# Performance work log

Hardware: AMD Instinct MI355X
Metric: run time of the kernel (lower is better)

The kernel has to match this reference:

```python
import jax, jax.numpy as jnp
import numpy as np

EPS_NORM = 1e-10
EPS_EXP = 1e-6


def setup_inputs() -> dict:
    key = jax.random.key(0)
    k1, k2 = jax.random.split(key)
    B, F, H, W = 16, 2048, 8, 8
    X = jax.random.normal(k1, (B, F, H, W), dtype=jnp.float32)
    M = jax.random.normal(k2, (B, F, H, W), dtype=jnp.float32)
    return {"X": X, "M": M}


def reference(X, M):
    B, F, H, W = X.shape
    N = H * W
    X = X.reshape(B, F, N)
    M = M.reshape(B, F, N)

    # feature centering over dim=-2 (the feature axis of (B, F, N))
    X = X - X.mean(axis=1, keepdims=True)
    M = M - M.mean(axis=1, keepdims=True)

    # feature_normalize: L2 norm over dim 1, keepdim, + eps
    X = X / (jnp.linalg.norm(X, axis=1, keepdims=True) + EPS_NORM)
    M = M / (jnp.linalg.norm(M, axis=1, keepdims=True) + EPS_NORM)

    # MatmulTopkLoss: S = X @ M^T over spatial N -> (B, F, F)
    S = jnp.einsum('bfn,bgn->bfg', X, M)
    YX = S + jnp.transpose(S, (0, 2, 1))  # symmetrize
    P = jax.nn.softmax(YX, axis=-1)

    k = F // 2
    value, idx = jax.lax.top_k(P, k)  # (B, F, k) values desc, indices
    value_sum = value.sum(axis=-1, keepdims=True)
    row_pos = jnp.arange(F)[None, :, None]  # (1, F, 1)
    dist = jnp.abs(idx - row_pos).astype(value.dtype)
    C_xy = (value * dist / value_sum).mean(axis=-1)  # (B, F)

    xy = jnp.exp(-C_xy + C_xy.min() - EPS_EXP)
    return jnp.reshape(xy.mean(), (1,))
```

## Files before the change

### kernel.cpp

```cpp
#include <hip/hip_runtime.h>
#include <hip/hip_bf16.h>
#include <math.h>

#define B_   16
#define F_   2048
#define N_   64
#define K_   1024
#define YP   2056

typedef short bf16x8 __attribute__((ext_vector_type(8)));
typedef float v4f    __attribute__((ext_vector_type(4)));

__device__ __forceinline__ float wave_sum(float v) {
#pragma unroll
  for (int off = 32; off > 0; off >>= 1) v += __shfl_down(v, off, 64);
  return v;
}
__device__ __forceinline__ float wave_max(float v) {
#pragma unroll
  for (int off = 32; off > 0; off >>= 1) v = fmaxf(v, __shfl_down(v, off, 64));
  return v;
}

__device__ __forceinline__ unsigned f2bf(float x) {
  const unsigned u = __float_as_uint(x);
  return (u + 0x7FFFu + ((u >> 16) & 1u)) >> 16;
}
__device__ __forceinline__ float bf2f(unsigned us) {
  return __uint_as_float(us << 16);
}
__device__ __forceinline__ unsigned ord2u16(unsigned T) {
  return (T & 0x8000u) ? (T ^ 0x8000u) : (T ^ 0xFFFFu);
}
__device__ __forceinline__ unsigned ordpair(unsigned wd) {
  return wd ^ (0x80008000u | (((wd & 0x80008000u) >> 15) * 0x7FFFu));
}

__global__ __launch_bounds__(256) void stats_kernel(
    const float* __restrict__ X, const float* __restrict__ M,
    float* __restrict__ P) {
  __shared__ float red[4][N_][4];
  const int tid = threadIdx.x;
  const int b = blockIdx.x >> 4;
  const int fb = blockIdx.x & 15;
  const int f0 = fb * 128;
  const int fi = tid >> 6, n = tid & 63;
  float sx = 0.f, sxx = 0.f, sm = 0.f, smm = 0.f;
#pragma unroll 4
  for (int j = 0; j < 32; ++j) {
    const int f = f0 + fi + 4 * j;
    const size_t gi = ((size_t)b * F_ + f) * N_ + n;
    const float x = X[gi];
    const float m = M[gi];
    sx += x; sxx += x * x; sm += m; smm += m * m;
  }
  red[fi][n][0] = sx; red[fi][n][1] = sxx;
  red[fi][n][2] = sm; red[fi][n][3] = smm;
  __syncthreads();
  const int wn = tid & 63, word = tid >> 6;
  const float s = red[0][wn][word] + red[1][wn][word] +
                  red[2][wn][word] + red[3][wn][word];
  P[(((size_t)b * N_ + wn) * 4 + word) * 16 + fb] = s;
}

__global__ __launch_bounds__(256) void normbf_kernel(
    const float* __restrict__ X, const float* __restrict__ M,
    const float* __restrict__ P,
    short* __restrict__ Xb16, short* __restrict__ Mb16) {
  const int tid = threadIdx.x;
  const int b = blockIdx.x >> 4;
  const int f0 = (blockIdx.x & 15) * 128;
  const int n = tid & 63;
  const float* base = P + (((size_t)b * N_ + n) * 4) * 16;
  float acc4[4];
#pragma unroll
  for (int wj = 0; wj < 4; ++wj) {
    float s = 0.f;
#pragma unroll
    for (int i = 0; i < 16; ++i) s += base[16 * wj + i];
    acc4[wj] = s;
  }
  const float sx = acc4[0], sxx = acc4[1], sm = acc4[2], smm = acc4[3];
  const float mux = sx * (1.f / F_), mum = sm * (1.f / F_);
  const float rx = 1.f / (sqrtf(fmaxf(sxx - (float)F_ * mux * mux, 0.f)) + 1e-10f);
  const float rm = 1.f / (sqrtf(fmaxf(smm - (float)F_ * mum * mum, 0.f)) + 1e-10f);
#pragma unroll 4
  for (int jj = 0; jj < 32; ++jj) {
    const int f = f0 + (tid >> 6) + 4 * jj;
    const size_t gi = ((size_t)b * F_ + f) * N_ + n;
    Xb16[gi] = (short)f2bf((X[gi] - mux) * rx);
    Mb16[gi] = (short)f2bf((M[gi] - mum) * rm);
  }
}

__global__ __launch_bounds__(512)
__attribute__((amdgpu_waves_per_eu(4, 4)))
void rows_kernel(
    const short* __restrict__ Xb16, const short* __restrict__ Mb16,
    float* __restrict__ C) {
  __shared__ unsigned short yxu[16 * YP];
  __shared__ unsigned histS[8 * 256];

  const int tid = threadIdx.x;
  const int w = tid >> 6, lane = tid & 63;
  const int nl = lane & 15, q = lane >> 4;
  const int b = blockIdx.x >> 7;
  const int f0 = (blockIdx.x & 127) * 16;
  const int g0 = 256 * w;

  const short* __restrict__ Xb = Xb16 + (size_t)b * F_ * N_;
  const short* __restrict__ Mb = Mb16 + (size_t)b * F_ * N_;

  const short* Ax = Xb + (size_t)(f0 + nl) * N_ + 8 * q;
  const short* Am = Mb + (size_t)(f0 + nl) * N_ + 8 * q;
  const bf16x8 ax0 = *(const bf16x8*)(Ax);
  const bf16x8 ax1 = *(const bf16x8*)(Ax + 32);
  const bf16x8 am0 = *(const bf16x8*)(Am);
  const bf16x8 am1 = *(const bf16x8*)(Am + 32);

  v4f acc[16];
#pragma unroll
  for (int t = 0; t < 16; ++t) acc[t] = (v4f)(0.f);

#pragma unroll
  for (int t = 0; t < 16; ++t) {
    const short* Bm = Mb + (size_t)(g0 + 16 * t + nl) * N_ + 8 * q;
    const short* Bx = Xb + (size_t)(g0 + 16 * t + nl) * N_ + 8 * q;
    const bf16x8 bm0 = *(const bf16x8*)(Bm);
    const bf16x8 bm1 = *(const bf16x8*)(Bm + 32);
    const bf16x8 bx0 = *(const bf16x8*)(Bx);
    const bf16x8 bx1 = *(const bf16x8*)(Bx + 32);
    acc[t] = __builtin_amdgcn_mfma_f32_16x16x32_bf16(ax0, bm0, acc[t], 0, 0, 0);
    acc[t] = __builtin_amdgcn_mfma_f32_16x16x32_bf16(ax1, bm1, acc[t], 0, 0, 0);
    acc[t] = __builtin_amdgcn_mfma_f32_16x16x32_bf16(am0, bx0, acc[t], 0, 0, 0);
    acc[t] = __builtin_amdgcn_mfma_f32_16x16x32_bf16(am1, bx1, acc[t], 0, 0, 0);
  }

#pragma unroll
  for (int t = 0; t < 16; ++t) {
    const int col = g0 + 16 * t + nl;
#pragma unroll
    for (int r = 0; r < 4; ++r)
      yxu[(4 * q + r) * YP + col] = (unsigned short)f2bf(acc[t][r]);
  }
  __syncthreads();

  unsigned* wh = &histS[w << 8];
#pragma unroll 1
  for (int r4 = 0; r4 < 2; ++r4) {
    const int row = 2 * w + r4;
    const int frow = f0 + row;
    const uint4* rp = (const uint4*)(yxu + row * YP);

    unsigned pk[16];
    unsigned kmin = 0xFFFFFFFFu, kmax = 0u;
#pragma unroll
    for (int j = 0; j < 4; ++j) {
      const uint4 tt = rp[lane + 64 * j];
      const unsigned wds[4] = {tt.x, tt.y, tt.z, tt.w};
#pragma unroll
      for (int c = 0; c < 4; ++c) {
        const unsigned o = ordpair(wds[c]);
        pk[4 * j + c] = o;
        const unsigned o0 = o & 0xFFFFu, o1 = o >> 16;
        kmin = min(kmin, min(o0, o1));
        kmax = max(kmax, max(o0, o1));
      }
    }
#pragma unroll
    for (int off = 32; off > 0; off >>= 1) {
      kmin = min(kmin, (unsigned)__shfl_down((int)kmin, off, 64));
      kmax = max(kmax, (unsigned)__shfl_down((int)kmax, off, 64));
    }
    kmin = (unsigned)__shfl((int)kmin, 0, 64);
    kmax = (unsigned)__shfl((int)kmax, 0, 64);

    unsigned lo = kmin, R = kmax - kmin, krem = K_;
    unsigned T, tie_need;
    if (R == 0) {
      T = lo; tie_need = krem;
    } else {
      for (;;) {
        const int pos = 31 - __builtin_clz(R);
        const int sh = (pos > 7) ? (pos - 7) : 0;
#pragma unroll
        for (int i = 0; i < 4; ++i) wh[lane + 64 * i] = 0u;
        __builtin_amdgcn_wave_barrier();
#pragma unroll
        for (int c = 0; c < 16; ++c) {
          const unsigned o = pk[c];
          const unsigned d0 = (o & 0xFFFFu) - lo;
          const unsigned d1 = (o >> 16) - lo;
          if (d0 <= R) atomicAdd(&wh[d0 >> sh], 1u);
          if (d1 <= R) atomicAdd(&wh[d1 >> sh], 1u);
        }
        __builtin_amdgcn_wave_barrier();
        unsigned h[4];
#pragma unroll
        for (int i = 0; i < 4; ++i) h[i] = wh[4 * lane + i];
        unsigned s3 = h[3], s2 = h[2] + s3, s1 = h[1] + s2, s0 = h[0] + s1;
        unsigned tot = s0;
#pragma unroll
        for (int off = 1; off < 64; off <<= 1) {
          const unsigned v = __shfl_down(tot, off, 64);
          if (lane + off < 64) tot += v;
        }
        const unsigned above = tot - s0;
        const unsigned S[4] = {above + s0, above + s1, above + s2, above + s3};
        unsigned packed = 0;
        bool found = false;
#pragma unroll
        for (int i = 0; i < 4; ++i) {
          const unsigned Sip1 = S[i] - h[i];
          if (S[i] >= krem && Sip1 < krem) {
            packed = ((unsigned)(4 * lane + i) << 16) | Sip1;
            found = true;
          }
        }
        const unsigned long long bm = __ballot(found);
        const int winner = __ffsll(bm) - 1;
        packed = (unsigned)__shfl((int)packed, winner, 64);
        const unsigned D = packed >> 16;
        krem -= (packed & 0xFFFFu);
        if (sh == 0) { T = lo + D; tie_need = krem; break; }
        lo += (D << sh);
        R = (1u << sh) - 1u;
      }
    }

    float vs = 0.f, ws = 0.f;
    unsigned cnt[4];
#pragma unroll
    for (int j = 0; j < 4; ++j) {
      cnt[j] = 0;
#pragma unroll
      for (int c = 0; c < 4; ++c) {
        const unsigned o = pk[4 * j + c];
        const unsigned oo[2] = {o & 0xFFFFu, o >> 16};
#pragma unroll
        for (int i = 0; i < 2; ++i) {
          const int g = 512 * j + 8 * lane + 2 * c + i;
          if (oo[i] > T) {
            const float pv = __expf(bf2f(ord2u16(oo[i])));
            vs += pv; ws += pv * fabsf((float)(g - frow));
          } else if (oo[i] == T) cnt[j]++;
        }
      }
    }
    const float ptie = __expf(bf2f(ord2u16(T)));

    unsigned pA = cnt[0] | (cnt[1] << 16), pB = cnt[2] | (cnt[3] << 16);
    unsigned iA = pA, iB = pB;
#pragma unroll
    for (int off = 1; off < 64; off <<= 1) {
      const unsigned vA = __shfl_up(iA, off, 64);
      const unsigned vB = __shfl_up(iB, off, 64);
      if (lane >= off) { iA += vA; iB += vB; }
    }
    const unsigned eA = iA - pA, eB = iB - pB;
    const unsigned tA = (unsigned)__shfl((int)iA, 63, 64);
    const unsigned tB = (unsigned)__shfl((int)iB, 63, 64);
    unsigned G[4];
    G[0] = 0;
    G[1] = G[0] + (tA & 0xFFFFu);
    G[2] = G[1] + (tA >> 16);
    G[3] = G[2] + (tB & 0xFFFFu);
#pragma unroll
    for (int j = 0; j < 4; ++j) {
      if (cnt[j]) {
        const unsigned off = (j < 2) ? ((eA >> (16 * j)) & 0xFFFFu)
                                     : ((eB >> (16 * (j - 2))) & 0xFFFFu);
        unsigned cc = 0;
#pragma unroll
        for (int c = 0; c < 4; ++c) {
          const unsigned o = pk[4 * j + c];
          const unsigned oo[2] = {o & 0xFFFFu, o >> 16};
#pragma unroll
          for (int i = 0; i < 2; ++i) {
            if (oo[i] == T) {
              if (G[j] + off + cc < tie_need) {
                const int g = 512 * j + 8 * lane + 2 * c + i;
                vs += ptie; ws += ptie * fabsf((float)(g - frow));
              }
              cc++;
            }
          }
        }
      }
    }

    vs = wave_sum(vs); ws = wave_sum(ws);
    if (lane == 0)
      C[(size_t)b * F_ + frow] = (ws / vs) * (1.f / (float)K_);
  }
}

__global__ __launch_bounds__(1024) void final_kernel(
    const float* __restrict__ C, unsigned* __restrict__ out) {
  __shared__ float red[16];
  const int tid = threadIdx.x;
  const int wave = tid >> 6, lane = tid & 63;
  float v[32];
  float mn = 3.4e38f;
#pragma unroll
  for (int i = 0; i < 32; ++i) {
    v[i] = C[tid + 1024 * i];
    mn = fminf(mn, v[i]);
  }
  mn = -wave_max(-mn);
  if (lane == 0) red[wave] = mn;
  __syncthreads();
  float cmin = red[0];
  for (int w = 1; w < 16; ++w) cmin = fminf(cmin, red[w]);
  __syncthreads();
  float s = 0.f;
#pragma unroll
  for (int i = 0; i < 32; ++i) s += expf(cmin - v[i] - 1e-6f);
  s = wave_sum(s);
  if (lane == 0) red[wave] = s;
  __syncthreads();
  if (tid == 0) {
    float tot = 0.f;
    for (int w = 0; w < 16; ++w) tot += red[w];
    const float res = tot * (1.f / 32768.f);
    const __hip_bfloat16 hb = __float2bfloat16(res);
    const unsigned short u = *(const unsigned short*)&hb;
    out[0] = ((unsigned)u << 16) | (unsigned)u;
  }
}

extern "C" void kernel_launch(void* const* d_in, const int* in_sizes, int n_in,
                              void* d_out, int out_size, void* d_ws, size_t ws_size,
                              hipStream_t stream) {
  const float* X = (const float*)d_in[0];
  const float* M = (const float*)d_in[1];
  short* Xb16 = (short*)d_ws;
  short* Mb16 = Xb16 + (size_t)B_ * F_ * N_;
  float* C = (float*)(Mb16 + (size_t)B_ * F_ * N_);
  float* P = C + (size_t)B_ * F_;

  stats_kernel<<<dim3(B_ * 16), dim3(256), 0, stream>>>(X, M, P);
  normbf_kernel<<<dim3(B_ * 16), dim3(256), 0, stream>>>(X, M, P, Xb16, Mb16);
  rows_kernel<<<dim3(B_ * (F_ / 16)), dim3(512), 0, stream>>>(Xb16, Mb16, C);
  final_kernel<<<dim3(1), dim3(1024), 0, stream>>>(C, (unsigned*)d_out);
}
```

Before: 230.8 us.

## Interleave row pairs in LDS and vectorize stats/normalize with float4 loads

The rows kernel now packs two adjacent output rows into one 32-bit LDS word per column, so each wave reads its two rows with a single pass of uint4 loads. It computes min/max for both rows at once, then runs the radix select on the low or high half. The stats and normalize kernels switch to float4 loads and 4-wide bf16 stores, and normalize computes per-column mean and inverse norm once into shared memory. The aim is fewer LDS and global transactions, at the cost of 32 packed registers per lane in the rows kernel, which may raise register pressure.

New measurement: 239.7 us. 1.04x slower.

```diff
diff --git a/kernel.cpp b/kernel.cpp
--- a/kernel.cpp
+++ b/kernel.cpp
@@ -6,10 +6,11 @@
 #define F_   2048
 #define N_   64
 #define K_   1024
-#define YP   2056
+#define YPW  2052
 
 typedef short bf16x8 __attribute__((ext_vector_type(8)));
 typedef float v4f    __attribute__((ext_vector_type(4)));
+typedef unsigned short u16x4 __attribute__((ext_vector_type(4)));
 
 __device__ __forceinline__ float wave_sum(float v) {
 #pragma unroll
@@ -39,57 +40,98 @@
 __global__ __launch_bounds__(256) void stats_kernel(
     const float* __restrict__ X, const float* __restrict__ M,
     float* __restrict__ P) {
-  __shared__ float red[4][N_][4];
-  const int tid = threadIdx.x;
+  __shared__ float4 red[4][16][16];
+  const int t = threadIdx.x;
   const int b = blockIdx.x >> 4;
   const int fb = blockIdx.x & 15;
-  const int f0 = fb * 128;
-  const int fi = tid >> 6, n = tid & 63;
-  float sx = 0.f, sxx = 0.f, sm = 0.f, smm = 0.f;
-#pragma unroll 4
-  for (int j = 0; j < 32; ++j) {
-    const int f = f0 + fi + 4 * j;
-    const size_t gi = ((size_t)b * F_ + f) * N_ + n;
-    const float x = X[gi];
-    const float m = M[gi];
-    sx += x; sxx += x * x; sm += m; smm += m * m;
-  }
-  red[fi][n][0] = sx; red[fi][n][1] = sxx;
-  red[fi][n][2] = sm; red[fi][n][3] = smm;
-  __syncthreads();
-  const int wn = tid & 63, word = tid >> 6;
-  const float s = red[0][wn][word] + red[1][wn][word] +
-                  red[2][wn][word] + red[3][wn][word];
-  P[(((size_t)b * N_ + wn) * 4 + word) * 16 + fb] = s;
+  const int nq = t & 15, fr = t >> 4;
+  const float4* __restrict__ X4 = (const float4*)X;
+  const float4* __restrict__ M4 = (const float4*)M;
+  float4 sx = make_float4(0.f, 0.f, 0.f, 0.f), sxx = sx, sm = sx, smm = sx;
+#pragma unroll
+  for (int it = 0; it < 8; ++it) {
+    const int f = fb * 128 + fr + 16 * it;
+    const size_t idx = ((size_t)b * F_ + f) * 16 + nq;
+    const float4 x = X4[idx];
+    const float4 m = M4[idx];
+    sx.x += x.x; sx.y += x.y; sx.z += x.z; sx.w += x.w;
+    sxx.x += x.x * x.x; sxx.y += x.y * x.y;
+    sxx.z += x.z * x.z; sxx.w += x.w * x.w;
+    sm.x += m.x; sm.y += m.y; sm.z += m.z; sm.w += m.w;
+    smm.x += m.x * m.x; smm.y += m.y * m.y;
+    smm.z += m.z * m.z; smm.w += m.w * m.w;
+  }
+  red[0][fr][nq] = sx; red[1][fr][nq] = sxx;
+  red[2][fr][nq] = sm; red[3][fr][nq] = smm;
+  __syncthreads();
+  const int n = t & 63, word = t >> 6;
+  const int q2 = n >> 2, sub = n & 3;
+  float s = 0.f;
+#pragma unroll
+  for (int f2 = 0; f2 < 16; ++f2) {
+    const float4 v = red[word][f2][q2];
+    s += (sub == 0) ? v.x : (sub == 1) ? v.y : (sub == 2) ? v.z : v.w;
+  }
+  P[(((size_t)b * N_ + n) * 4 + word) * 16 + fb] = s;
 }
 
 __global__ __launch_bounds__(256) void normbf_kernel(
     const float* __restrict__ X, const float* __restrict__ M,
     const float* __restrict__ P,
     short* __restrict__ Xb16, short* __restrict__ Mb16) {
-  const int tid = threadIdx.x;
+  __shared__ float der[N_][4];
+  __shared__ float sums[N_][4];
+  const int t = threadIdx.x;
   const int b = blockIdx.x >> 4;
   const int f0 = (blockIdx.x & 15) * 128;
-  const int n = tid & 63;
-  const float* base = P + (((size_t)b * N_ + n) * 4) * 16;
-  float acc4[4];
-#pragma unroll
-  for (int wj = 0; wj < 4; ++wj) {
+  {
+    const int n = t & 63, word = t >> 6;
+    const float* base = P + (((size_t)b * N_ + n) * 4 + word) * 16;
     float s = 0.f;
 #pragma unroll
-    for (int i = 0; i < 16; ++i) s += base[16 * wj + i];
-    acc4[wj] = s;
-  }
-  const float sx = acc4[0], sxx = acc4[1], sm = acc4[2], smm = acc4[3];
-  const float mux = sx * (1.f / F_), mum = sm * (1.f / F_);
-  const float rx = 1.f / (sqrtf(fmaxf(sxx - (float)F_ * mux * mux, 0.f)) + 1e-10f);
-  const float rm = 1.f / (sqrtf(fmaxf(smm - (float)F_ * mum * mum, 0.f)) + 1e-10f);
-#pragma unroll 4
-  for (int jj = 0; jj < 32; ++jj) {
-    const int f = f0 + (tid >> 6) + 4 * jj;
-    const size_t gi = ((size_t)b * F_ + f) * N_ + n;
-    Xb16[gi] = (short)f2bf((X[gi] - mux) * rx);
-    Mb16[gi] = (short)f2bf((M[gi] - mum) * rm);
+    for (int i = 0; i < 16; ++i) s += base[i];
+    sums[n][word] = s;
+  }
+  __syncthreads();
+  if (t < 128) {
+    const int n = t & 63, half = t >> 6;
+    const float sv = sums[n][2 * half], sq = sums[n][2 * half + 1];
+    const float mu = sv * (1.f / F_);
+    const float r = 1.f / (sqrtf(fmaxf(sq - (float)F_ * mu * mu, 0.f)) + 1e-10f);
+    der[n][2 * half] = mu;
+    der[n][2 * half + 1] = r;
+  }
+  __syncthreads();
+  const int nq = t & 15, fr = t >> 4;
+  const float mx0 = der[4 * nq + 0][0], rx0 = der[4 * nq + 0][1];
+  const float mx1 = der[4 * nq + 1][0], rx1 = der[4 * nq + 1][1];
+  const float mx2 = der[4 * nq + 2][0], rx2 = der[4 * nq + 2][1];
+  const float mx3 = der[4 * nq + 3][0], rx3 = der[4 * nq + 3][1];
+  const float mm0 = der[4 * nq + 0][2], rm0 = der[4 * nq + 0][3];
+  const float mm1 = der[4 * nq + 1][2], rm1 = der[4 * nq + 1][3];
+  const float mm2 = der[4 * nq + 2][2], rm2 = der[4 * nq + 2][3];
+  const float mm3 = der[4 * nq + 3][2], rm3 = der[4 * nq + 3][3];
+  const float4* __restrict__ X4 = (const float4*)X;
+  const float4* __restrict__ M4 = (const float4*)M;
+  u16x4* __restrict__ Xo = (u16x4*)Xb16;
+  u16x4* __restrict__ Mo = (u16x4*)Mb16;
+#pragma unroll
+  for (int it = 0; it < 8; ++it) {
+    const int f = f0 + fr + 16 * it;
+    const size_t idx = ((size_t)b * F_ + f) * 16 + nq;
+    const float4 x = X4[idx];
+    const float4 m = M4[idx];
+    u16x4 ox, om;
+    ox[0] = (unsigned short)f2bf((x.x - mx0) * rx0);
+    ox[1] = (unsigned short)f2bf((x.y - mx1) * rx1);
+    ox[2] = (unsigned short)f2bf((x.z - mx2) * rx2);
+    ox[3] = (unsigned short)f2bf((x.w - mx3) * rx3);
+    om[0] = (unsigned short)f2bf((m.x - mm0) * rm0);
+    om[1] = (unsigned short)f2bf((m.y - mm1) * rm1);
+    om[2] = (unsigned short)f2bf((m.z - mm2) * rm2);
+    om[3] = (unsigned short)f2bf((m.w - mm3) * rm3);
+    Xo[idx] = ox;
+    Mo[idx] = om;
   }
 }
 
@@ -98,7 +140,7 @@
 void rows_kernel(
     const short* __restrict__ Xb16, const short* __restrict__ Mb16,
     float* __restrict__ C) {
-  __shared__ unsigned short yxu[16 * YP];
+  __shared__ unsigned yxP32[8 * YPW];
   __shared__ unsigned histS[8 * 256];
 
   const int tid = threadIdx.x;
@@ -139,23 +181,20 @@
 #pragma unroll
   for (int t = 0; t < 16; ++t) {
     const int col = g0 + 16 * t + nl;
-#pragma unroll
-    for (int r = 0; r < 4; ++r)
-      yxu[(4 * q + r) * YP + col] = (unsigned short)f2bf(acc[t][r]);
+    const unsigned d0 = f2bf(acc[t][0]) | (f2bf(acc[t][1]) << 16);
+    const unsigned d1 = f2bf(acc[t][2]) | (f2bf(acc[t][3]) << 16);
+    yxP32[(2 * q) * YPW + col] = d0;
+    yxP32[(2 * q + 1) * YPW + col] = d1;
   }
   __syncthreads();
 
   unsigned* wh = &histS[w << 8];
-#pragma unroll 1
-  for (int r4 = 0; r4 < 2; ++r4) {
-    const int row = 2 * w + r4;
-    const int frow = f0 + row;
-    const uint4* rp = (const uint4*)(yxu + row * YP);
-
-    unsigned pk[16];
-    unsigned kmin = 0xFFFFFFFFu, kmax = 0u;
-#pragma unroll
-    for (int j = 0; j < 4; ++j) {
+  unsigned pk[32];
+  unsigned kmin0 = 0xFFFFFFFFu, kmax0 = 0u, kmin1 = 0xFFFFFFFFu, kmax1 = 0u;
+  {
+    const uint4* rp = (const uint4*)(yxP32 + w * YPW);
+#pragma unroll
+    for (int j = 0; j < 8; ++j) {
       const uint4 tt = rp[lane + 64 * j];
       const unsigned wds[4] = {tt.x, tt.y, tt.z, tt.w};
 #pragma unroll
@@ -163,17 +202,29 @@
         const unsigned o = ordpair(wds[c]);
         pk[4 * j + c] = o;
         const unsigned o0 = o & 0xFFFFu, o1 = o >> 16;
-        kmin = min(kmin, min(o0, o1));
-        kmax = max(kmax, max(o0, o1));
+        kmin0 = min(kmin0, o0); kmax0 = max(kmax0, o0);
+        kmin1 = min(kmin1, o1); kmax1 = max(kmax1, o1);
       }
     }
 #pragma unroll
     for (int off = 32; off > 0; off >>= 1) {
-      kmin = min(kmin, (unsigned)__shfl_down((int)kmin, off, 64));
-      kmax = max(kmax, (unsigned)__shfl_down((int)kmax, off, 64));
-    }
-    kmin = (unsigned)__shfl((int)kmin, 0, 64);
-    kmax = (unsigned)__shfl((int)kmax, 0, 64);
+      kmin0 = min(kmin0, (unsigned)__shfl_down((int)kmin0, off, 64));
+      kmax0 = max(kmax0, (unsigned)__shfl_down((int)kmax0, off, 64));
+      kmin1 = min(kmin1, (unsigned)__shfl_down((int)kmin1, off, 64));
+      kmax1 = max(kmax1, (unsigned)__shfl_down((int)kmax1, off, 64));
+    }
+    kmin0 = (unsigned)__shfl((int)kmin0, 0, 64);
+    kmax0 = (unsigned)__shfl((int)kmax0, 0, 64);
+    kmin1 = (unsigned)__shfl((int)kmin1, 0, 64);
+    kmax1 = (unsigned)__shfl((int)kmax1, 0, 64);
+  }
+
+#pragma unroll 1
+  for (int r4 = 0; r4 < 2; ++r4) {
+    const int frow = f0 + 2 * w + r4;
+    const int sh16 = 16 * r4;
+    const unsigned kmin = r4 ? kmin1 : kmin0;
+    const unsigned kmax = r4 ? kmax1 : kmax0;
 
     unsigned lo = kmin, R = kmax - kmin, krem = K_;
     unsigned T, tie_need;
@@ -187,12 +238,9 @@
         for (int i = 0; i < 4; ++i) wh[lane + 64 * i] = 0u;
         __builtin_amdgcn_wave_barrier();
 #pragma unroll
-        for (int c = 0; c < 16; ++c) {
-          const unsigned o = pk[c];
-          const unsigned d0 = (o & 0xFFFFu) - lo;
-          const unsigned d1 = (o >> 16) - lo;
-          if (d0 <= R) atomicAdd(&wh[d0 >> sh], 1u);
-          if (d1 <= R) atomicAdd(&wh[d1 >> sh], 1u);
+        for (int c = 0; c < 32; ++c) {
+          const unsigned d = ((pk[c] >> sh16) & 0xFFFFu) - lo;
+          if (d <= R) atomicAdd(&wh[d >> sh], 1u);
         }
         __builtin_amdgcn_wave_barrier();
         unsigned h[4];
@@ -229,61 +277,63 @@
     }
 
     float vs = 0.f, ws = 0.f;
-    unsigned cnt[4];
-#pragma unroll
-    for (int j = 0; j < 4; ++j) {
+    unsigned cnt[8];
+#pragma unroll
+    for (int j = 0; j < 8; ++j) {
       cnt[j] = 0;
 #pragma unroll
       for (int c = 0; c < 4; ++c) {
-        const unsigned o = pk[4 * j + c];
-        const unsigned oo[2] = {o & 0xFFFFu, o >> 16};
-#pragma unroll
-        for (int i = 0; i < 2; ++i) {
-          const int g = 512 * j + 8 * lane + 2 * c + i;
-          if (oo[i] > T) {
-            const float pv = __expf(bf2f(ord2u16(oo[i])));
-            vs += pv; ws += pv * fabsf((float)(g - frow));
-          } else if (oo[i] == T) cnt[j]++;
-        }
+        const unsigned key = (pk[4 * j + c] >> sh16) & 0xFFFFu;
+        const int g = 256 * j + 4 * lane + c;
+        if (key > T) {
+          const float pv = __expf(bf2f(ord2u16(key)));
+          vs += pv; ws += pv * fabsf((float)(g - frow));
+        } else if (key == T) cnt[j]++;
       }
     }
     const float ptie = __expf(bf2f(ord2u16(T)));
 
-    unsigned pA = cnt[0] | (cnt[1] << 16), pB = cnt[2] | (cnt[3] << 16);
-    unsigned iA = pA, iB = pB;
+    unsigned sw[4];
+#pragma unroll
+    for (int k2 = 0; k2 < 4; ++k2) sw[k2] = cnt[2 * k2] | (cnt[2 * k2 + 1] << 16);
+    unsigned iw[4] = {sw[0], sw[1], sw[2], sw[3]};
 #pragma unroll
     for (int off = 1; off < 64; off <<= 1) {
-      const unsigned vA = __shfl_up(iA, off, 64);
-      const unsigned vB = __shfl_up(iB, off, 64);
-      if (lane >= off) { iA += vA; iB += vB; }
-    }
-    const unsigned eA = iA - pA, eB = iB - pB;
-    const unsigned tA = (unsigned)__shfl((int)iA, 63, 64);
-    const unsigned tB = (unsigned)__shfl((int)iB, 63, 64);
-    unsigned G[4];
+      const unsigned v0 = __shfl_up(iw[0], off, 64);
+      const unsigned v1 = __shfl_up(iw[1], off, 64);
+      const unsigned v2 = __shfl_up(iw[2], off, 64);
+      const unsigned v3 = __shfl_up(iw[3], off, 64);
+      if (lane >= off) { iw[0] += v0; iw[1] += v1; iw[2] += v2; iw[3] += v3; }
+    }
+    unsigned ew[4], tw[4];
+#pragma unroll
+    for (int k2 = 0; k2 < 4; ++k2) {
+      ew[k2] = iw[k2] - sw[k2];
+      tw[k2] = (unsigned)__shfl((int)iw[k2], 63, 64);
+    }
+    unsigned G[8];
     G[0] = 0;
-    G[1] = G[0] + (tA & 0xFFFFu);
-    G[2] = G[1] + (tA >> 16);
-    G[3] = G[2] + (tB & 0xFFFFu);
-#pragma unroll
-    for (int j = 0; j < 4; ++j) {
+    G[1] = G[0] + (tw[0] & 0xFFFFu);
+    G[2] = G[1] + (tw[0] >> 16);
+    G[3] = G[2] + (tw[1] & 0xFFFFu);
+    G[4] = G[3] + (tw[1] >> 16);
+    G[5] = G[4] + (tw[2] & 0xFFFFu);
+    G[6] = G[5] + (tw[2] >> 16);
+    G[7] = G[6] + (tw[3] & 0xFFFFu);
+#pragma unroll
+    for (int j = 0; j < 8; ++j) {
       if (cnt[j]) {
-        const unsigned off = (j < 2) ? ((eA >> (16 * j)) & 0xFFFFu)
-                                     : ((eB >> (16 * (j - 2))) & 0xFFFFu);
+        const unsigned off = (ew[j >> 1] >> (16 * (j & 1))) & 0xFFFFu;
         unsigned cc = 0;
 #pragma unroll
         for (int c = 0; c < 4; ++c) {
-          const unsigned o = pk[4 * j + c];
-          const unsigned oo[2] = {o & 0xFFFFu, o >> 16};
-#pragma unroll
-          for (int i = 0; i < 2; ++i) {
-            if (oo[i] == T) {
-              if (G[j] + off + cc < tie_need) {
-                const int g = 512 * j + 8 * lane + 2 * c + i;
-                vs += ptie; ws += ptie * fabsf((float)(g - frow));
-              }
-              cc++;
+          const unsigned key = (pk[4 * j + c] >> sh16) & 0xFFFFu;
+          if (key == T) {
+            if (G[j] + off + cc < tie_need) {
+              const int g = 256 * j + 4 * lane + c;
+              vs += ptie; ws += ptie * fabsf((float)(g - frow));
             }
+            cc++;
           }
         }
       }
```

## Widen stats/normalize grids and fold final reduction into rows kernel via last-block counter

Applied to the files above, without the earlier changes.

Splits the stats and normalize kernels into four times as many blocks (32 features each instead of 128) so more CUs share the memory-bound pre-pass. The normalize kernel now reduces the partial sums cooperatively in shared memory with float4 loads instead of every thread summing all partials. The single-block final kernel is removed, and the last rows_kernel block to finish (found with an atomic counter reset in stats_kernel) does the min/exp-mean reduction. This saves one launch at the cost of an atomic and threadfence per block and a serial tail reduction on 512 threads.

Result: slower. 494.7 us (+114.3%).

```diff
diff --git a/kernel.cpp b/kernel.cpp
--- a/kernel.cpp
+++ b/kernel.cpp
@@ -38,16 +38,17 @@
 
 __global__ __launch_bounds__(256) void stats_kernel(
     const float* __restrict__ X, const float* __restrict__ M,
-    float* __restrict__ P) {
+    float* __restrict__ P, unsigned* __restrict__ counter) {
   __shared__ float red[4][N_][4];
+  if (blockIdx.x == 0 && threadIdx.x == 0) *counter = 0u;
   const int tid = threadIdx.x;
-  const int b = blockIdx.x >> 4;
-  const int fb = blockIdx.x & 15;
-  const int f0 = fb * 128;
+  const int b = blockIdx.x >> 6;
+  const int fb = blockIdx.x & 63;
+  const int f0 = fb * 32;
   const int fi = tid >> 6, n = tid & 63;
   float sx = 0.f, sxx = 0.f, sm = 0.f, smm = 0.f;
-#pragma unroll 4
-  for (int j = 0; j < 32; ++j) {
+#pragma unroll
+  for (int j = 0; j < 8; ++j) {
     const int f = f0 + fi + 4 * j;
     const size_t gi = ((size_t)b * F_ + f) * N_ + n;
     const float x = X[gi];
@@ -60,33 +61,46 @@
   const int wn = tid & 63, word = tid >> 6;
   const float s = red[0][wn][word] + red[1][wn][word] +
                   red[2][wn][word] + red[3][wn][word];
-  P[(((size_t)b * N_ + wn) * 4 + word) * 16 + fb] = s;
+  P[(((size_t)b * N_ + wn) * 4 + word) * 64 + fb] = s;
 }
 
 __global__ __launch_bounds__(256) void normbf_kernel(
     const float* __restrict__ X, const float* __restrict__ M,
     const float* __restrict__ P,
     short* __restrict__ Xb16, short* __restrict__ Mb16) {
-  const int tid = threadIdx.x;
-  const int b = blockIdx.x >> 4;
-  const int f0 = (blockIdx.x & 15) * 128;
-  const int n = tid & 63;
-  const float* base = P + (((size_t)b * N_ + n) * 4) * 16;
-  float acc4[4];
-#pragma unroll
-  for (int wj = 0; wj < 4; ++wj) {
-    float s = 0.f;
-#pragma unroll
-    for (int i = 0; i < 16; ++i) s += base[16 * wj + i];
-    acc4[wj] = s;
-  }
-  const float sx = acc4[0], sxx = acc4[1], sm = acc4[2], smm = acc4[3];
-  const float mux = sx * (1.f / F_), mum = sm * (1.f / F_);
-  const float rx = 1.f / (sqrtf(fmaxf(sxx - (float)F_ * mux * mux, 0.f)) + 1e-10f);
-  const float rm = 1.f / (sqrtf(fmaxf(smm - (float)F_ * mum * mum, 0.f)) + 1e-10f);
-#pragma unroll 4
-  for (int jj = 0; jj < 32; ++jj) {
-    const int f = f0 + (tid >> 6) + 4 * jj;
+  __shared__ float der[N_][4];
+  __shared__ float sums[N_][4];
+  const int t = threadIdx.x;
+  const int b = blockIdx.x >> 6;
+  const int f0 = (blockIdx.x & 63) * 32;
+  {
+    const int n = t & 63, word = t >> 6;
+    const float4* base =
+        (const float4*)(P + (((size_t)b * N_ + n) * 4 + word) * 64);
+    float4 a = make_float4(0.f, 0.f, 0.f, 0.f);
+#pragma unroll
+    for (int i = 0; i < 16; ++i) {
+      const float4 v = base[i];
+      a.x += v.x; a.y += v.y; a.z += v.z; a.w += v.w;
+    }
+    sums[n][word] = a.x + a.y + a.z + a.w;
+  }
+  __syncthreads();
+  if (t < 128) {
+    const int n = t & 63, half = t >> 6;
+    const float sv = sums[n][2 * half], sq = sums[n][2 * half + 1];
+    const float mu = sv * (1.f / F_);
+    const float r = 1.f / (sqrtf(fmaxf(sq - (float)F_ * mu * mu, 0.f)) + 1e-10f);
+    der[n][2 * half] = mu;
+    der[n][2 * half + 1] = r;
+  }
+  __syncthreads();
+  const int n = t & 63;
+  const float mux = der[n][0], rx = der[n][1];
+  const float mum = der[n][2], rm = der[n][3];
+#pragma unroll
+  for (int jj = 0; jj < 8; ++jj) {
+    const int f = f0 + (t >> 6) + 4 * jj;
     const size_t gi = ((size_t)b * F_ + f) * N_ + n;
     Xb16[gi] = (short)f2bf((X[gi] - mux) * rx);
     Mb16[gi] = (short)f2bf((M[gi] - mum) * rm);
@@ -97,9 +111,12 @@
 __attribute__((amdgpu_waves_per_eu(4, 4)))
 void rows_kernel(
     const short* __restrict__ Xb16, const short* __restrict__ Mb16,
-    float* __restrict__ C) {
+    float* __restrict__ C, unsigned* __restrict__ counter,
+    unsigned* __restrict__ out) {
   __shared__ unsigned short yxu[16 * YP];
   __shared__ unsigned histS[8 * 256];
+  __shared__ float fred[8];
+  __shared__ unsigned isLast;
 
   const int tid = threadIdx.x;
   const int w = tid >> 6, lane = tid & 63;
@@ -293,35 +310,31 @@
     if (lane == 0)
       C[(size_t)b * F_ + frow] = (ws / vs) * (1.f / (float)K_);
   }
-}
-
-__global__ __launch_bounds__(1024) void final_kernel(
-    const float* __restrict__ C, unsigned* __restrict__ out) {
-  __shared__ float red[16];
-  const int tid = threadIdx.x;
-  const int wave = tid >> 6, lane = tid & 63;
-  float v[32];
+
+  __threadfence();
+  if (tid == 0) isLast = (atomicAdd(counter, 1u) == (unsigned)(gridDim.x - 1));
+  __syncthreads();
+  if (!isLast) return;
+  __threadfence();
+  volatile const float* Cv = C;
   float mn = 3.4e38f;
-#pragma unroll
-  for (int i = 0; i < 32; ++i) {
-    v[i] = C[tid + 1024 * i];
-    mn = fminf(mn, v[i]);
-  }
+  for (int i = tid; i < B_ * F_; i += 512) mn = fminf(mn, Cv[i]);
   mn = -wave_max(-mn);
-  if (lane == 0) red[wave] = mn;
-  __syncthreads();
-  float cmin = red[0];
-  for (int w = 1; w < 16; ++w) cmin = fminf(cmin, red[w]);
+  if (lane == 0) fred[w] = mn;
+  __syncthreads();
+  float cmin = fred[0];
+#pragma unroll
+  for (int i = 1; i < 8; ++i) cmin = fminf(cmin, fred[i]);
   __syncthreads();
   float s = 0.f;
-#pragma unroll
-  for (int i = 0; i < 32; ++i) s += expf(cmin - v[i] - 1e-6f);
+  for (int i = tid; i < B_ * F_; i += 512) s += expf(cmin - Cv[i] - 1e-6f);
   s = wave_sum(s);
-  if (lane == 0) red[wave] = s;
+  if (lane == 0) fred[w] = s;
   __syncthreads();
   if (tid == 0) {
     float tot = 0.f;
-    for (int w = 0; w < 16; ++w) tot += red[w];
+#pragma unroll
+    for (int i = 0; i < 8; ++i) tot += fred[i];
     const float res = tot * (1.f / 32768.f);
     const __hip_bfloat16 hb = __float2bfloat16(res);
     const unsigned short u = *(const unsigned short*)&hb;
@@ -338,9 +351,10 @@
   short* Mb16 = Xb16 + (size_t)B_ * F_ * N_;
   float* C = (float*)(Mb16 + (size_t)B_ * F_ * N_);
   float* P = C + (size_t)B_ * F_;
-
-  stats_kernel<<<dim3(B_ * 16), dim3(256), 0, stream>>>(X, M, P);
-  normbf_kernel<<<dim3(B_ * 16), dim3(256), 0, stream>>>(X, M, P, Xb16, Mb16);
-  rows_kernel<<<dim3(B_ * (F_ / 16)), dim3(512), 0, stream>>>(Xb16, Mb16, C);
-  final_kernel<<<dim3(1), dim3(1024), 0, stream>>>(C, (unsigned*)d_out);
-}
+  unsigned* counter = (unsigned*)(P + (size_t)B_ * N_ * 4 * 64);
+
+  stats_kernel<<<dim3(B_ * 64), dim3(256), 0, stream>>>(X, M, P, counter);
+  normbf_kernel<<<dim3(B_ * 64), dim3(256), 0, stream>>>(X, M, P, Xb16, Mb16);
+  rows_kernel<<<dim3(B_ * (F_ / 16)), dim3(512), 0, stream>>>(
+      Xb16, Mb16, C, counter, (unsigned*)d_out);
+}
```
